# Optimization experiments

Measured on AMD Instinct MI355X. Metric: run time of the kernel, lower is better.

Reference implementation:

```python
import jax, jax.numpy as jnp
import numpy as np

M = 3.96875  # 127/32: clamp bound of the 8-bit-ish fixed-point format


def fix_x(x, m=M):
    # STE quantize: floor(x*32)/32 in forward, identity grad; then exact clamp to [-m, m]
    x = x * 32
    pos = jax.nn.relu(x)
    pos = pos - jax.lax.stop_gradient(pos) + jnp.floor(pos)
    neg = jax.nn.relu(-x)
    neg = neg - jax.lax.stop_gradient(neg) + jnp.ceil(neg)
    x = (pos - neg) / 32
    pos = m - jax.nn.relu(m - jax.nn.relu(x))
    neg = m - jax.nn.relu(m - jax.nn.relu(-x))
    return pos - neg


def setup_inputs() -> dict:
    key = jax.random.key(0)
    k1, k2, k3 = jax.random.split(key, 3)
    B, OUT, IN = 32, 1024, 1024
    x = jax.random.normal(k1, (B, OUT, IN), dtype=jnp.float32)
    weight = jax.random.normal(k2, (OUT, IN), dtype=jnp.float32) * 0.05
    bias = jax.random.normal(k3, (OUT,), dtype=jnp.float32) * 0.05
    return {"x": x, "weight": weight, "bias": bias}


def reference(x, weight, bias):
    # elementwise product then fake-quant: [B, OUT, IN]
    x = fix_x(x * weight)
    dim3 = x.shape[2]
    # Serial (non-associative) quantized suffix reduction along last axis:
    # acc <- fix_x(x[..., k] + acc) for k = dim3-2 ... 0, acc init = x[..., -1].
    init = x[:, :, -1]                                   # [B, OUT]
    xs = jnp.moveaxis(x[:, :, : dim3 - 1], -1, 0)[::-1]  # [IN-1, B, OUT]

    def step(carry, s):
        return fix_x(s + carry), None

    acc, _ = jax.lax.scan(step, init, xs)                # [B, OUT]
    out = fix_x(acc[:, None, :])                         # [B, 1, OUT]
    out = fix_x(out + bias)
    return out
```

## Files before the change

### kernel.cpp

```cpp
#include <hip/hip_runtime.h>
#include <math.h>


#define IN_DIM  1024
#define OUT_DIM 1024
#define B_DIM   32

typedef float vfloat4 __attribute__((ext_vector_type(4)));

__global__ __launch_bounds__(256) void ffl_kernel(
    const float* __restrict__ x,
    const float* __restrict__ w,
    const float* __restrict__ bias,
    float* __restrict__ out)
{
    const int lane = threadIdx.x & 63;
    const int wid  = threadIdx.x >> 6;

    const int xcd = blockIdx.x & 7;
    const int j   = blockIdx.x >> 3;
    const int o   = (xcd << 7) | (j >> 3);
    const int b   = (((j & 7) << 2) | wid);

    const vfloat4* xp = (const vfloat4*)(x + ((size_t)b * OUT_DIM + o) * IN_DIM + lane * 16);
    const vfloat4* wp = (const vfloat4*)(w + (size_t)o * IN_DIM + lane * 16);

    int rs = 0;
    int rL = -(1 << 28);
    int rU =  (1 << 28);

    #pragma unroll
    for (int jj = 0; jj < 4; ++jj) {
        vfloat4 xv = xp[jj];
        vfloat4 wv = wp[jj];
        float pe[4] = { xv.x * wv.x, xv.y * wv.y, xv.z * wv.z, xv.w * wv.w };
        #pragma unroll
        for (int e = 0; e < 4; ++e) {
            float t = floorf(pe[e] * 32.0f);
            t = fminf(fmaxf(t, -127.0f), 127.0f);
            int v = (int)t;
            bool isInit = (jj == 3) && (e == 3) && (lane == 63);
            int sE = isInit ? 0 : v;
            int LE = isInit ? v : -127;
            int UE = isInit ? v : 127;
            int ns = sE + rs;
            int nL = min(max(LE + rs, rL), rU);
            int nU = min(max(UE + rs, rL), rU);
            rs = ns; rL = nL; rU = nU;
        }
    }

    #pragma unroll
    for (int m = 1; m < 64; m <<= 1) {
        int ps = __shfl_xor(rs, m, 64);
        int pL = __shfl_xor(rL, m, 64);
        int pU = __shfl_xor(rU, m, 64);
        bool lower = ((lane & m) == 0);
        int sG = lower ? rs : ps;
        int LG = lower ? rL : pL;
        int UG = lower ? rU : pU;
        int sF = lower ? ps : rs;
        int LF = lower ? pL : rL;
        int UF = lower ? pU : rU;
        rs = sF + sG;
        rL = min(max(LF + sG, LG), UG);
        rU = min(max(UF + sG, LG), UG);
    }

    if (lane == 0) {
        float acc = (float)rL * 0.03125f;
        float tb  = acc + bias[o];
        float r   = floorf(tb * 32.0f);
        r = fminf(fmaxf(r, -127.0f), 127.0f);
        out[(size_t)b * OUT_DIM + o] = r * 0.03125f;
    }
}

extern "C" void kernel_launch(void* const* d_in, const int* in_sizes, int n_in,
                              void* d_out, int out_size, void* d_ws, size_t ws_size,
                              hipStream_t stream) {
    const float* x    = (const float*)d_in[0];
    const float* w    = (const float*)d_in[1];
    const float* bias = (const float*)d_in[2];
    float* out = (float*)d_out;

    const int pairs  = B_DIM * OUT_DIM;
    const int blocks = pairs / 4;
    ffl_kernel<<<blocks, 256, 0, stream>>>(x, w, bias, out);
}
```

Before: 195.8 us.

## Split each row across a full block and combine wave partials in shared memory

After: 194.0 us. About the same (-1.0%).

```diff
diff --git a/kernel.cpp b/kernel.cpp
--- a/kernel.cpp
+++ b/kernel.cpp
@@ -19,35 +19,34 @@
 
     const int xcd = blockIdx.x & 7;
     const int j   = blockIdx.x >> 3;
-    const int o   = (xcd << 7) | (j >> 3);
-    const int b   = (((j & 7) << 2) | wid);
+    const int o   = (xcd << 7) | (j >> 5);
+    const int b   = j & 31;
 
-    const vfloat4* xp = (const vfloat4*)(x + ((size_t)b * OUT_DIM + o) * IN_DIM + lane * 16);
-    const vfloat4* wp = (const vfloat4*)(w + (size_t)o * IN_DIM + lane * 16);
+    const size_t rowx = ((size_t)b * OUT_DIM + o) * IN_DIM;
+    const size_t roww = (size_t)o * IN_DIM;
+    const int    off  = (wid << 8) + (lane << 2);
+
+    vfloat4 xv = *(const vfloat4*)(x + rowx + off);
+    vfloat4 wv = *(const vfloat4*)(w + roww + off);
 
     int rs = 0;
     int rL = -(1 << 28);
     int rU =  (1 << 28);
 
+    float pe[4] = { xv.x * wv.x, xv.y * wv.y, xv.z * wv.z, xv.w * wv.w };
     #pragma unroll
-    for (int jj = 0; jj < 4; ++jj) {
-        vfloat4 xv = xp[jj];
-        vfloat4 wv = wp[jj];
-        float pe[4] = { xv.x * wv.x, xv.y * wv.y, xv.z * wv.z, xv.w * wv.w };
-        #pragma unroll
-        for (int e = 0; e < 4; ++e) {
-            float t = floorf(pe[e] * 32.0f);
-            t = fminf(fmaxf(t, -127.0f), 127.0f);
-            int v = (int)t;
-            bool isInit = (jj == 3) && (e == 3) && (lane == 63);
-            int sE = isInit ? 0 : v;
-            int LE = isInit ? v : -127;
-            int UE = isInit ? v : 127;
-            int ns = sE + rs;
-            int nL = min(max(LE + rs, rL), rU);
-            int nU = min(max(UE + rs, rL), rU);
-            rs = ns; rL = nL; rU = nU;
-        }
+    for (int e = 0; e < 4; ++e) {
+        float t = floorf(pe[e] * 32.0f);
+        t = fminf(fmaxf(t, -127.0f), 127.0f);
+        int v = (int)t;
+        bool isInit = (wid == 3) && (lane == 63) && (e == 3);
+        int sE = isInit ? 0 : v;
+        int LE = isInit ? v : -127;
+        int UE = isInit ? v : 127;
+        int ns = sE + rs;
+        int nL = min(max(LE + rs, rL), rU);
+        int nU = min(max(UE + rs, rL), rU);
+        rs = ns; rL = nL; rU = nU;
     }
 
     #pragma unroll
@@ -67,8 +66,20 @@
         rU = min(max(UF + sG, LG), UG);
     }
 
-    if (lane == 0) {
-        float acc = (float)rL * 0.03125f;
+    __shared__ int Ss[4], Sl[4], Su[4];
+    if (lane == 0) { Ss[wid] = rs; Sl[wid] = rL; Su[wid] = rU; }
+    __syncthreads();
+
+    if (threadIdx.x == 0) {
+        int cs = Ss[3], cL = Sl[3], cU = Su[3];
+        #pragma unroll
+        for (int k = 2; k >= 0; --k) {
+            int sG = Ss[k], LG = Sl[k], UG = Su[k];
+            int nL = min(max(cL + sG, LG), UG);
+            int nU = min(max(cU + sG, LG), UG);
+            cs = cs + sG; cL = nL; cU = nU;
+        }
+        float acc = (float)cL * 0.03125f;
         float tb  = acc + bias[o];
         float r   = floorf(tb * 32.0f);
         r = fminf(fmaxf(r, -127.0f), 127.0f);
@@ -84,7 +95,6 @@
     const float* bias = (const float*)d_in[2];
     float* out = (float*)d_out;
 
-    const int pairs  = B_DIM * OUT_DIM;
-    const int blocks = pairs / 4;
+    const int blocks = B_DIM * OUT_DIM;
     ffl_kernel<<<blocks, 256, 0, stream>>>(x, w, bias, out);
 }
```
